# Kernel optimization log

Measured on AMD Instinct MI355X. Metric: run time of the kernel, lower is better.

Reference implementation:

```python
import jax, jax.numpy as jnp
import numpy as np
from jax.scipy.special import logsumexp

V, K, E, HD = 30000, 17, 128, 256
H = HD // 2  # per-direction hidden = 128
B, T = 128, 512


def setup_inputs() -> dict:
    key = jax.random.key(0)
    ks = jax.random.split(key, 16)
    s_e = 1.0 / np.sqrt(H)
    return {
        "input_ids": jax.random.randint(ks[0], (B, T), 0, V, dtype=jnp.int32),
        "tags": jax.random.randint(ks[1], (B, T), 0, K, dtype=jnp.int32),
        "mask": jnp.ones((B, T), dtype=bool),
        "embed_table": jax.random.normal(ks[2], (V, E), jnp.float32),
        "w_ih_f": jax.random.uniform(ks[3], (4 * H, E), jnp.float32, -s_e, s_e),
        "w_hh_f": jax.random.uniform(ks[4], (4 * H, H), jnp.float32, -s_e, s_e),
        "b_ih_f": jax.random.uniform(ks[5], (4 * H,), jnp.float32, -s_e, s_e),
        "b_hh_f": jax.random.uniform(ks[6], (4 * H,), jnp.float32, -s_e, s_e),
        "w_ih_b": jax.random.uniform(ks[7], (4 * H, E), jnp.float32, -s_e, s_e),
        "w_hh_b": jax.random.uniform(ks[8], (4 * H, H), jnp.float32, -s_e, s_e),
        "b_ih_b": jax.random.uniform(ks[9], (4 * H,), jnp.float32, -s_e, s_e),
        "b_hh_b": jax.random.uniform(ks[10], (4 * H,), jnp.float32, -s_e, s_e),
        "w_emit": jax.random.uniform(ks[11], (K, HD), jnp.float32, -s_e, s_e),
        "b_emit": jax.random.uniform(ks[12], (K,), jnp.float32, -s_e, s_e),
        "start_trans": jax.random.uniform(ks[13], (K,), jnp.float32, -0.1, 0.1),
        "end_trans": jax.random.uniform(ks[14], (K,), jnp.float32, -0.1, 0.1),
        "trans": jax.random.uniform(ks[15], (K, K), jnp.float32, -0.1, 0.1),
    }


def _lstm_dir(x, w_ih, w_hh, b_ih, b_hh):
    # x: [T, B, E] -> hs: [T, B, H]; PyTorch gate order i, f, g, o
    xp = jnp.einsum('tbe,ge->tbg', x, w_ih) + b_ih + b_hh  # [T,B,4H]
    h0 = jnp.zeros((x.shape[1], H), x.dtype)

    def step(carry, xpt):
        h, c = carry
        gates = xpt + h @ w_hh.T
        i, f, g, o = jnp.split(gates, 4, axis=-1)
        c = jax.nn.sigmoid(f) * c + jax.nn.sigmoid(i) * jnp.tanh(g)
        h = jax.nn.sigmoid(o) * jnp.tanh(c)
        return (h, c), h

    _, hs = jax.lax.scan(step, (h0, h0), xp)
    return hs


def _crf_nll_mean(emissions, tags, mask, start_trans, end_trans, trans):
    # emissions [B,T,K], tags [B,T] int, mask [B,T] bool; torchcrf reduction='mean'
    em_t = jnp.transpose(emissions, (1, 0, 2))      # [T,B,K]
    tags_t = tags.T                                  # [T,B]
    mask_t = mask.T                                  # [T,B]
    b_idx = jnp.arange(emissions.shape[0])
    mf = mask_t.astype(emissions.dtype)

    # numerator: score of the gold path
    score0 = start_trans[tags_t[0]] + em_t[0, b_idx, tags_t[0]]

    def num_step(carry, inp):
        score, prev = carry
        em, tg, m, mb = inp
        s = trans[prev, tg] + em[b_idx, tg]
        score = score + s * m
        prev = jnp.where(mb, tg, prev)
        return (score, prev), None

    (score, last_tag), _ = jax.lax.scan(
        num_step, (score0, tags_t[0]), (em_t[1:], tags_t[1:], mf[1:], mask_t[1:]))
    score = score + end_trans[last_tag]

    # denominator: forward algorithm (log partition)
    alpha0 = start_trans[None, :] + em_t[0]  # [B,K]

    def den_step(alpha, inp):
        em, mb = inp
        nxt = logsumexp(alpha[:, :, None] + trans[None, :, :] + em[:, None, :], axis=1)
        return jnp.where(mb[:, None], nxt, alpha), None

    alpha, _ = jax.lax.scan(den_step, alpha0, (em_t[1:], mask_t[1:]))
    logZ = logsumexp(alpha + end_trans[None, :], axis=1)

    llh = score - logZ
    return -jnp.mean(llh)


def reference(input_ids, tags, mask, embed_table,
              w_ih_f, w_hh_f, b_ih_f, b_hh_f,
              w_ih_b, w_hh_b, b_ih_b, b_hh_b,
              w_emit, b_emit, start_trans, end_trans, trans):
    x = embed_table[input_ids]                 # [B,T,E]
    xt = jnp.transpose(x, (1, 0, 2))           # [T,B,E]
    hs_f = _lstm_dir(xt, w_ih_f, w_hh_f, b_ih_f, b_hh_f)
    hs_b = _lstm_dir(xt[::-1], w_ih_b, w_hh_b, b_ih_b, b_hh_b)[::-1]
    h = jnp.concatenate([hs_f, hs_b], axis=-1)  # [T,B,2H]
    h = jnp.transpose(h, (1, 0, 2))             # [B,T,2H]
    emissions = jnp.einsum('bth,kh->btk', h, w_emit) + b_emit
    return _crf_nll_mean(emissions, tags, mask, start_trans, end_trans, trans)
```

## Files before the change

kernel.cpp:

```cpp
#include <hip/hip_runtime.h>
#include <hip/hip_bf16.h>


typedef __attribute__((ext_vector_type(8))) short short8;
typedef __attribute__((ext_vector_type(4))) float f32x4;
typedef __fp16 h2 __attribute__((ext_vector_type(2)));

__device__ __forceinline__ float bf2f(unsigned short u) {
    return __uint_as_float(((unsigned int)u) << 16);
}
__device__ __forceinline__ unsigned short f2bf(float f) {
    unsigned int x = __float_as_uint(f);
    x += 0x7FFFu + ((x >> 16) & 1u);
    return (unsigned short)(x >> 16);
}
__device__ __forceinline__ float sigf(float x) {
    return __builtin_amdgcn_rcpf(1.f + __expf(-x));
}
__device__ __forceinline__ float tanhf_(float x) {
    float e = __expf(-2.f * fabsf(x));
    float t = (1.f - e) * __builtin_amdgcn_rcpf(1.f + e);
    return copysignf(t, x);
}
__device__ __forceinline__ h2 i2h2(int x) { h2 r; __builtin_memcpy(&r, &x, 4); return r; }
__device__ __forceinline__ int h22i(h2 x) { int r; __builtin_memcpy(&r, &x, 4); return r; }

__device__ __forceinline__ float dot2acc(h2 a, h2 b, float c) {
#if __has_builtin(__builtin_amdgcn_fdot2)
    return __builtin_amdgcn_fdot2(a, b, c, false);
#else
    return fmaf((float)a.x, (float)b.x, fmaf((float)a.y, (float)b.y, c));
#endif
}

__global__ __launch_bounds__(256) void xp_gemm(
    const int* __restrict__ ids, const float* __restrict__ emb,
    const float* __restrict__ w_ih_f, const float* __restrict__ w_ih_b,
    const float* __restrict__ b_ih_f, const float* __restrict__ b_hh_f,
    const float* __restrict__ b_ih_b, const float* __restrict__ b_hh_b,
    unsigned short* __restrict__ xp)
{
    __shared__ unsigned short Ab[128][136];
    __shared__ unsigned short Wb[64][136];
    __shared__ unsigned short Cb[128][72];

    const int tid = threadIdx.x;
    const int m0  = blockIdx.x * 128;
    const int t   = m0 >> 7;

    {
        const int r = tid >> 1, half = tid & 1;
        const int id = ids[r * 512 + t];
        const float4* src = (const float4*)(emb + (long)id * 128 + half * 64);
        #pragma unroll
        for (int j = 0; j < 16; ++j) {
            float4 v = src[j];
            unsigned int p0 = (unsigned int)f2bf(v.x) | ((unsigned int)f2bf(v.y) << 16);
            unsigned int p1 = (unsigned int)f2bf(v.z) | ((unsigned int)f2bf(v.w) << 16);
            *(unsigned int*)&Ab[r][half*64 + j*4]     = p0;
            *(unsigned int*)&Ab[r][half*64 + j*4 + 2] = p1;
        }
    }

    const int w  = tid >> 6, l = tid & 63;
    const int lr = l & 15,  lg = l >> 4;

    for (int it = 0; it < 16; ++it) {
        const int n0 = it * 64;
        __syncthreads();
        {
            const int r = tid >> 2, q = tid & 3;
            const int g = n0 + r;
            const float* srcw = (g < 512) ? (w_ih_f + (long)g * 128)
                                          : (w_ih_b + (long)(g - 512) * 128);
            const float4* s4 = (const float4*)(srcw + q * 32);
            #pragma unroll
            for (int j = 0; j < 8; ++j) {
                float4 v = s4[j];
                unsigned int p0 = (unsigned int)f2bf(v.x) | ((unsigned int)f2bf(v.y) << 16);
                unsigned int p1 = (unsigned int)f2bf(v.z) | ((unsigned int)f2bf(v.w) << 16);
                *(unsigned int*)&Wb[r][q*32 + j*4]     = p0;
                *(unsigned int*)&Wb[r][q*32 + j*4 + 2] = p1;
            }
        }
        __syncthreads();

        f32x4 acc[2][4];
        #pragma unroll
        for (int a = 0; a < 2; ++a)
            #pragma unroll
            for (int c = 0; c < 4; ++c)
                acc[a][c] = (f32x4){0.f, 0.f, 0.f, 0.f};

        #pragma unroll
        for (int kk = 0; kk < 4; ++kk) {
            const int kb = kk * 32 + lg * 8;
            short8 af[2], bfr[4];
            #pragma unroll
            for (int mt2 = 0; mt2 < 2; ++mt2)
                af[mt2] = *(const short8*)&Ab[w*32 + mt2*16 + lr][kb];
            #pragma unroll
            for (int nt2 = 0; nt2 < 4; ++nt2)
                bfr[nt2] = *(const short8*)&Wb[nt2*16 + lr][kb];
            #pragma unroll
            for (int mt2 = 0; mt2 < 2; ++mt2)
                #pragma unroll
                for (int nt2 = 0; nt2 < 4; ++nt2)
                    acc[mt2][nt2] = __builtin_amdgcn_mfma_f32_16x16x32_bf16(
                        af[mt2], bfr[nt2], acc[mt2][nt2], 0, 0, 0);
        }

        #pragma unroll
        for (int nt2 = 0; nt2 < 4; ++nt2) {
            const int gc = n0 + nt2*16 + lr;
            const float bv = (gc < 512) ? (b_ih_f[gc] + b_hh_f[gc])
                                        : (b_ih_b[gc-512] + b_hh_b[gc-512]);
            #pragma unroll
            for (int mt2 = 0; mt2 < 2; ++mt2) {
                #pragma unroll
                for (int r = 0; r < 4; ++r) {
                    const int lrow = w*32 + mt2*16 + lg*4 + r;
                    Cb[lrow][nt2*16 + lr] = f2bf(acc[mt2][nt2][r] + bv);
                }
            }
        }
        __syncthreads();

        {
            const int rr = tid >> 1, hf = tid & 1;
            const int grow = m0 + rr;
            long dst;
            if (n0 < 512) {
                dst = (long)grow * 512 + n0 + hf*32;
            } else {
                const int tt = grow >> 7, bb = grow & 127;
                dst = 33554432L + (long)((511 - tt) * 128 + bb) * 512 + (n0 - 512) + hf*32;
            }
            const unsigned short* srcC = &Cb[rr][hf*32];
            unsigned short* dp = xp + dst;
            #pragma unroll
            for (int j = 0; j < 4; ++j)
                *(short8*)(dp + j*8) = *(const short8*)(srcC + j*8);
        }
    }
}

__global__ __launch_bounds__(256, 1) void lstm_rec(
    const unsigned short* __restrict__ xp,
    const float* __restrict__ w_hh_f, const float* __restrict__ w_hh_b,
    unsigned short* __restrict__ hbuf)
{
    const int tid = threadIdx.x;
    const int dir = blockIdx.x >> 7, b = blockIdx.x & 127;
    const float* whh = dir ? w_hh_b : w_hh_f;

    h2 w1p[64], w2p[64];
    #pragma unroll
    for (int j = 0; j < 16; ++j) {
        float4 a = *(const float4*)(whh + (long)tid * 128 + j*8);
        float4 c = *(const float4*)(whh + (long)tid * 128 + j*8 + 4);
        w1p[j*4+0] = __builtin_amdgcn_cvt_pkrtz(a.x, a.y);
        w1p[j*4+1] = __builtin_amdgcn_cvt_pkrtz(a.z, a.w);
        w1p[j*4+2] = __builtin_amdgcn_cvt_pkrtz(c.x, c.y);
        w1p[j*4+3] = __builtin_amdgcn_cvt_pkrtz(c.z, c.w);
    }
    #pragma unroll
    for (int j = 0; j < 16; ++j) {
        float4 a = *(const float4*)(whh + (long)(tid + 256) * 128 + j*8);
        float4 c = *(const float4*)(whh + (long)(tid + 256) * 128 + j*8 + 4);
        w2p[j*4+0] = __builtin_amdgcn_cvt_pkrtz(a.x, a.y);
        w2p[j*4+1] = __builtin_amdgcn_cvt_pkrtz(a.z, a.w);
        w2p[j*4+2] = __builtin_amdgcn_cvt_pkrtz(c.x, c.y);
        w2p[j*4+3] = __builtin_amdgcn_cvt_pkrtz(c.z, c.w);
    }

    __shared__ float gl[4][128];
    const int l   = tid & 63;
    const int u   = tid & 127;
    const int grp = tid >> 7;

    int hpi = 0;
    float cv0 = 0.f, cv1 = 0.f;
    const unsigned short* xpd = xp + (long)dir * 33554432L;

    unsigned short nxa = xpd[((long)0 * 128 + b) * 512 + tid];
    unsigned short nxb = xpd[((long)0 * 128 + b) * 512 + tid + 256];

    for (int t = 0; t < 512; ++t) {
        const float xpv1 = bf2f(nxa);
        const float xpv2 = bf2f(nxb);
        if (t < 511) {
            const unsigned short* nr = xpd + ((long)(t+1) * 128 + b) * 512;
            nxa = nr[tid];
            nxb = nr[tid + 256];
        }

        float acc1 = 0.f, acc2 = 0.f;
        #pragma unroll
        for (int j = 0; j < 64; ++j) {
            const h2 hj = i2h2(__builtin_amdgcn_readlane(hpi, j));
            acc1 = dot2acc(w1p[j], hj, acc1);
            acc2 = dot2acc(w2p[j], hj, acc2);
        }

        gl[grp][u]     = acc1 + xpv1;
        gl[2 + grp][u] = acc2 + xpv2;
        __syncthreads();

        const float2 iv = *(const float2*)&gl[0][2*l];
        const float2 fv = *(const float2*)&gl[1][2*l];
        const float2 gv = *(const float2*)&gl[2][2*l];
        const float2 ov = *(const float2*)&gl[3][2*l];
        cv0 = sigf(fv.x) * cv0 + sigf(iv.x) * tanhf_(gv.x);
        cv1 = sigf(fv.y) * cv1 + sigf(iv.y) * tanhf_(gv.y);
        const float h0 = sigf(ov.x) * tanhf_(cv0);
        const float h1 = sigf(ov.y) * tanhf_(cv1);
        hpi = h22i(__builtin_amdgcn_cvt_pkrtz(h0, h1));

        if (tid < 64) {
            const int tt = dir ? (511 - t) : t;
            unsigned short* hd = hbuf + ((long)b * 512 + tt) * 256 + dir * 128;
            *(unsigned int*)&hd[2*l] =
                (unsigned int)f2bf(h0) | ((unsigned int)f2bf(h1) << 16);
        }
        __syncthreads();
    }
}

__global__ __launch_bounds__(256) void emission(
    const unsigned short* __restrict__ hbuf, const float* __restrict__ w_emit,
    const float* __restrict__ b_emit, float* __restrict__ em)
{
    const int tid = threadIdx.x, w = tid >> 6, l = tid & 63;
    const int lr = l & 15, lg = l >> 4;
    const int m0 = blockIdx.x * 128;

    short8 bf[2][8];
    #pragma unroll
    for (int nt = 0; nt < 2; ++nt) {
        const int col = nt*16 + lr;
        #pragma unroll
        for (int kk = 0; kk < 8; ++kk) {
            short8 v = (short8){0,0,0,0,0,0,0,0};
            if (col < 17) {
                const float* s = w_emit + (long)col * 256 + kk*32 + lg*8;
                const float4 a = *(const float4*)s;
                const float4 c = *(const float4*)(s + 4);
                v[0] = (short)f2bf(a.x); v[1] = (short)f2bf(a.y);
                v[2] = (short)f2bf(a.z); v[3] = (short)f2bf(a.w);
                v[4] = (short)f2bf(c.x); v[5] = (short)f2bf(c.y);
                v[6] = (short)f2bf(c.z); v[7] = (short)f2bf(c.w);
            }
            bf[nt][kk] = v;
        }
    }

    f32x4 acc[2][2];
    #pragma unroll
    for (int a = 0; a < 2; ++a)
        #pragma unroll
        for (int c = 0; c < 2; ++c)
            acc[a][c] = (f32x4){0.f, 0.f, 0.f, 0.f};

    #pragma unroll
    for (int kk = 0; kk < 8; ++kk) {
        short8 af[2];
        #pragma unroll
        for (int mt = 0; mt < 2; ++mt) {
            const long row = m0 + w*32 + mt*16 + lr;
            af[mt] = *(const short8*)(hbuf + row * 256 + kk*32 + lg*8);
        }
        #pragma unroll
        for (int mt = 0; mt < 2; ++mt)
            #pragma unroll
            for (int nt = 0; nt < 2; ++nt)
                acc[mt][nt] = __builtin_amdgcn_mfma_f32_16x16x32_bf16(
                    af[mt], bf[nt][kk], acc[mt][nt], 0, 0, 0);
    }

    #pragma unroll
    for (int mt = 0; mt < 2; ++mt)
        #pragma unroll
        for (int nt = 0; nt < 2; ++nt) {
            const int col = nt*16 + lr;
            if (col < 17) {
                const float bb = b_emit[col];
                #pragma unroll
                for (int r = 0; r < 4; ++r) {
                    const long row = m0 + w*32 + mt*16 + lg*4 + r;
                    em[row * 17 + col] = acc[mt][nt][r] + bb;
                }
            }
        }
}

__global__ __launch_bounds__(64) void crf(
    const float* __restrict__ em, const int* __restrict__ tags,
    const float* __restrict__ start_t, const float* __restrict__ end_t,
    const float* __restrict__ trans, float* __restrict__ llh)
{
    const int b = blockIdx.x, l = threadIdx.x;
    const int* tg = tags + b * 512;
    const float* emb_ = em + (long)b * 512 * 17;

    float sc = 0.f;
    #pragma unroll
    for (int it = 0; it < 8; ++it) {
        const int t = it * 64 + l;
        const int cur = tg[t];
        float e = emb_[t * 17 + cur];
        float tr = (t > 0) ? trans[tg[t-1] * 17 + cur] : 0.f;
        sc += e + tr;
    }
    #pragma unroll
    for (int m = 32; m >= 1; m >>= 1) sc += __shfl_xor(sc, m, 64);

    const bool act = (l < 17);
    const int j = act ? l : 16;

    float eT[17];
    #pragma unroll
    for (int i = 0; i < 17; ++i) eT[i] = __expf(trans[i * 17 + j]);

    float v0 = act ? (start_t[j] + emb_[j]) : -1e30f;
    float m0 = v0;
    #pragma unroll
    for (int m = 32; m >= 1; m >>= 1) m0 = fmaxf(m0, __shfl_xor(m0, m, 64));
    float al = act ? __expf(v0 - m0) : 0.f;
    float accl = m0;

    float em_next = emb_[17 + j];
    for (int t = 1; t < 512; ++t) {
        const float emv = em_next;
        if (t + 1 < 512) em_next = emb_[(t + 1) * 17 + j];
        float s = 0.f;
        #pragma unroll
        for (int i = 0; i < 17; ++i) {
            const float ai = __int_as_float(
                __builtin_amdgcn_readlane(__float_as_int(al), i));
            s = fmaf(ai, eT[i], s);
        }
        al = act ? s * __expf(emv) : 0.f;
        if ((t & 3) == 0) {
            float mx = al;
            #pragma unroll
            for (int m = 32; m >= 1; m >>= 1) mx = fmaxf(mx, __shfl_xor(mx, m, 64));
            al = al * __builtin_amdgcn_rcpf(mx);
            accl += __logf(mx);
        }
    }
    float fin = act ? al * __expf(end_t[j]) : 0.f;
    #pragma unroll
    for (int m = 32; m >= 1; m >>= 1) fin += __shfl_xor(fin, m, 64);
    const float logZ = __logf(fin) + accl;

    if (l == 0) {
        sc += start_t[tg[0]] + end_t[tg[511]];
        llh[b] = sc - logZ;
    }
}

__global__ __launch_bounds__(64) void finalize(
    const float* __restrict__ llh, float* __restrict__ out)
{
    const int l = threadIdx.x;
    float s = llh[l] + llh[l + 64];
    #pragma unroll
    for (int m = 32; m >= 1; m >>= 1) s += __shfl_xor(s, m, 64);
    if (l == 0) out[0] = -s * (1.f / 128.f);
}

extern "C" void kernel_launch(void* const* d_in, const int* in_sizes, int n_in,
                              void* d_out, int out_size, void* d_ws, size_t ws_size,
                              hipStream_t stream) {
    (void)in_sizes; (void)n_in; (void)out_size; (void)ws_size;
    const int*   ids    = (const int*)d_in[0];
    const int*   tags   = (const int*)d_in[1];
    const float* emb    = (const float*)d_in[3];
    const float* w_ih_f = (const float*)d_in[4];
    const float* w_hh_f = (const float*)d_in[5];
    const float* b_ih_f = (const float*)d_in[6];
    const float* b_hh_f = (const float*)d_in[7];
    const float* w_ih_b = (const float*)d_in[8];
    const float* w_hh_b = (const float*)d_in[9];
    const float* b_ih_b = (const float*)d_in[10];
    const float* b_hh_b = (const float*)d_in[11];
    const float* w_emit = (const float*)d_in[12];
    const float* b_emit = (const float*)d_in[13];
    const float* st     = (const float*)d_in[14];
    const float* en     = (const float*)d_in[15];
    const float* tr     = (const float*)d_in[16];

    char* ws = (char*)d_ws;
    unsigned short* xp   = (unsigned short*)(ws);
    unsigned short* hbuf = (unsigned short*)(ws + 134217728L);
    float*          em   = (float*)(ws + 167772160L);
    float*          llh  = (float*)(ws + 172228608L);
    float*          out  = (float*)d_out;

    xp_gemm<<<dim3(512), dim3(256), 0, stream>>>(ids, emb, w_ih_f, w_ih_b,
                                                 b_ih_f, b_hh_f, b_ih_b, b_hh_b, xp);
    lstm_rec<<<dim3(256), dim3(256), 0, stream>>>(xp, w_hh_f, w_hh_b, hbuf);
    emission<<<dim3(512), dim3(256), 0, stream>>>(hbuf, w_emit, b_emit, em);
    crf<<<dim3(128), dim3(64), 0, stream>>>(em, tags, st, en, tr, llh);
    finalize<<<dim3(1), dim3(64), 0, stream>>>(llh, out);
}
```

Measured before the change: 816.2 us.

## Pack two LSTM sequences per block and double-buffer gate LDS to drop a barrier

The recurrent LSTM kernel now runs two independent sequences per 512-thread block (128 blocks instead of 256) and double-buffers the shared gate array by timestep parity. This lets it remove the second __syncthreads per step. The aim is to halve the barriers per step and use fewer CUs. The trade-off is that the two sequences' waves now wait on each other at every barrier, and launch_bounds(512,2) may constrain the register budget for the 128 packed weights per thread.

```diff
diff --git a/kernel.cpp b/kernel.cpp
--- a/kernel.cpp
+++ b/kernel.cpp
@@ -145,20 +145,23 @@
     }
 }
 
-__global__ __launch_bounds__(256, 1) void lstm_rec(
+__global__ __launch_bounds__(512, 2) void lstm_rec(
     const unsigned short* __restrict__ xp,
     const float* __restrict__ w_hh_f, const float* __restrict__ w_hh_b,
     unsigned short* __restrict__ hbuf)
 {
-    const int tid = threadIdx.x;
-    const int dir = blockIdx.x >> 7, b = blockIdx.x & 127;
+    const int tid  = threadIdx.x;
+    const int s    = tid >> 8;
+    const int stid = tid & 255;
+    const int seq  = blockIdx.x * 2 + s;
+    const int dir  = seq >> 7, b = seq & 127;
     const float* whh = dir ? w_hh_b : w_hh_f;
 
     h2 w1p[64], w2p[64];
     #pragma unroll
     for (int j = 0; j < 16; ++j) {
-        float4 a = *(const float4*)(whh + (long)tid * 128 + j*8);
-        float4 c = *(const float4*)(whh + (long)tid * 128 + j*8 + 4);
+        float4 a = *(const float4*)(whh + (long)stid * 128 + j*8);
+        float4 c = *(const float4*)(whh + (long)stid * 128 + j*8 + 4);
         w1p[j*4+0] = __builtin_amdgcn_cvt_pkrtz(a.x, a.y);
         w1p[j*4+1] = __builtin_amdgcn_cvt_pkrtz(a.z, a.w);
         w1p[j*4+2] = __builtin_amdgcn_cvt_pkrtz(c.x, c.y);
@@ -166,33 +169,34 @@
     }
     #pragma unroll
     for (int j = 0; j < 16; ++j) {
-        float4 a = *(const float4*)(whh + (long)(tid + 256) * 128 + j*8);
-        float4 c = *(const float4*)(whh + (long)(tid + 256) * 128 + j*8 + 4);
+        float4 a = *(const float4*)(whh + (long)(stid + 256) * 128 + j*8);
+        float4 c = *(const float4*)(whh + (long)(stid + 256) * 128 + j*8 + 4);
         w2p[j*4+0] = __builtin_amdgcn_cvt_pkrtz(a.x, a.y);
         w2p[j*4+1] = __builtin_amdgcn_cvt_pkrtz(a.z, a.w);
         w2p[j*4+2] = __builtin_amdgcn_cvt_pkrtz(c.x, c.y);
         w2p[j*4+3] = __builtin_amdgcn_cvt_pkrtz(c.z, c.w);
     }
 
-    __shared__ float gl[4][128];
-    const int l   = tid & 63;
-    const int u   = tid & 127;
-    const int grp = tid >> 7;
+    __shared__ float gl[2][2][4][128];
+    const int l   = stid & 63;
+    const int u   = stid & 127;
+    const int grp = stid >> 7;
 
     int hpi = 0;
     float cv0 = 0.f, cv1 = 0.f;
     const unsigned short* xpd = xp + (long)dir * 33554432L;
 
-    unsigned short nxa = xpd[((long)0 * 128 + b) * 512 + tid];
-    unsigned short nxb = xpd[((long)0 * 128 + b) * 512 + tid + 256];
+    unsigned short nxa = xpd[((long)0 * 128 + b) * 512 + stid];
+    unsigned short nxb = xpd[((long)0 * 128 + b) * 512 + stid + 256];
 
     for (int t = 0; t < 512; ++t) {
+        const int p = t & 1;
         const float xpv1 = bf2f(nxa);
         const float xpv2 = bf2f(nxb);
         if (t < 511) {
             const unsigned short* nr = xpd + ((long)(t+1) * 128 + b) * 512;
-            nxa = nr[tid];
-            nxb = nr[tid + 256];
+            nxa = nr[stid];
+            nxb = nr[stid + 256];
         }
 
         float acc1 = 0.f, acc2 = 0.f;
@@ -203,27 +207,26 @@
             acc2 = dot2acc(w2p[j], hj, acc2);
         }
 
-        gl[grp][u]     = acc1 + xpv1;
-        gl[2 + grp][u] = acc2 + xpv2;
+        gl[s][p][grp][u]     = acc1 + xpv1;
+        gl[s][p][2 + grp][u] = acc2 + xpv2;
         __syncthreads();
 
-        const float2 iv = *(const float2*)&gl[0][2*l];
-        const float2 fv = *(const float2*)&gl[1][2*l];
-        const float2 gv = *(const float2*)&gl[2][2*l];
-        const float2 ov = *(const float2*)&gl[3][2*l];
+        const float2 iv = *(const float2*)&gl[s][p][0][2*l];
+        const float2 fv = *(const float2*)&gl[s][p][1][2*l];
+        const float2 gv = *(const float2*)&gl[s][p][2][2*l];
+        const float2 ov = *(const float2*)&gl[s][p][3][2*l];
         cv0 = sigf(fv.x) * cv0 + sigf(iv.x) * tanhf_(gv.x);
         cv1 = sigf(fv.y) * cv1 + sigf(iv.y) * tanhf_(gv.y);
         const float h0 = sigf(ov.x) * tanhf_(cv0);
         const float h1 = sigf(ov.y) * tanhf_(cv1);
         hpi = h22i(__builtin_amdgcn_cvt_pkrtz(h0, h1));
 
-        if (tid < 64) {
+        if (stid < 64) {
             const int tt = dir ? (511 - t) : t;
             unsigned short* hd = hbuf + ((long)b * 512 + tt) * 256 + dir * 128;
             *(unsigned int*)&hd[2*l] =
                 (unsigned int)f2bf(h0) | ((unsigned int)f2bf(h1) << 16);
         }
-        __syncthreads();
     }
 }
 
@@ -400,7 +403,7 @@
 
     xp_gemm<<<dim3(512), dim3(256), 0, stream>>>(ids, emb, w_ih_f, w_ih_b,
                                                  b_ih_f, b_hh_f, b_ih_b, b_hh_b, xp);
-    lstm_rec<<<dim3(256), dim3(256), 0, stream>>>(xp, w_hh_f, w_hh_b, hbuf);
+    lstm_rec<<<dim3(128), dim3(512), 0, stream>>>(xp, w_hh_f, w_hh_b, hbuf);
     emission<<<dim3(512), dim3(256), 0, stream>>>(hbuf, w_emit, b_emit, em);
     crf<<<dim3(128), dim3(64), 0, stream>>>(em, tags, st, en, tr, llh);
     finalize<<<dim3(1), dim3(64), 0, stream>>>(llh, out);
```

Result: slower. 985.5 us (+20.7%).

## Double-buffer LSTM gate exchange to drop one barrier per timestep

Applied to the files above, without the earlier changes.

The recurrent LSTM kernel now ping-pongs the shared gate buffer across timesteps, which removes the second __syncthreads per step. It also changes the hidden-unit ownership (lane l handles units l and l+64) and packs the weights to match, so all four gates of a unit sit in one float4 slot. The dot-product loop uses two accumulators per output to shorten the dependency chain, and the launch-bounds occupancy hint is raised to 2. In exchange, hbuf is written with two scalar 16-bit stores instead of one 32-bit store, and the higher occupancy hint may limit registers for the 128 packed weights per thread.

```diff
diff --git a/kernel.cpp b/kernel.cpp
--- a/kernel.cpp
+++ b/kernel.cpp
@@ -145,7 +145,7 @@
     }
 }
 
-__global__ __launch_bounds__(256, 1) void lstm_rec(
+__global__ __launch_bounds__(256, 2) void lstm_rec(
     const unsigned short* __restrict__ xp,
     const float* __restrict__ w_hh_f, const float* __restrict__ w_hh_b,
     unsigned short* __restrict__ hbuf)
@@ -156,37 +156,39 @@
 
     h2 w1p[64], w2p[64];
     #pragma unroll
-    for (int j = 0; j < 16; ++j) {
-        float4 a = *(const float4*)(whh + (long)tid * 128 + j*8);
-        float4 c = *(const float4*)(whh + (long)tid * 128 + j*8 + 4);
-        w1p[j*4+0] = __builtin_amdgcn_cvt_pkrtz(a.x, a.y);
-        w1p[j*4+1] = __builtin_amdgcn_cvt_pkrtz(a.z, a.w);
-        w1p[j*4+2] = __builtin_amdgcn_cvt_pkrtz(c.x, c.y);
-        w1p[j*4+3] = __builtin_amdgcn_cvt_pkrtz(c.z, c.w);
-    }
-    #pragma unroll
-    for (int j = 0; j < 16; ++j) {
-        float4 a = *(const float4*)(whh + (long)(tid + 256) * 128 + j*8);
-        float4 c = *(const float4*)(whh + (long)(tid + 256) * 128 + j*8 + 4);
-        w2p[j*4+0] = __builtin_amdgcn_cvt_pkrtz(a.x, a.y);
-        w2p[j*4+1] = __builtin_amdgcn_cvt_pkrtz(a.z, a.w);
-        w2p[j*4+2] = __builtin_amdgcn_cvt_pkrtz(c.x, c.y);
-        w2p[j*4+3] = __builtin_amdgcn_cvt_pkrtz(c.z, c.w);
-    }
-
-    __shared__ float gl[4][128];
-    const int l   = tid & 63;
-    const int u   = tid & 127;
-    const int grp = tid >> 7;
-
+    for (int jj = 0; jj < 16; ++jj) {
+        float4 a = *(const float4*)(whh + (long)tid * 128 + jj*4);
+        float4 c = *(const float4*)(whh + (long)tid * 128 + 64 + jj*4);
+        w1p[jj*4+0] = __builtin_amdgcn_cvt_pkrtz(a.x, c.x);
+        w1p[jj*4+1] = __builtin_amdgcn_cvt_pkrtz(a.y, c.y);
+        w1p[jj*4+2] = __builtin_amdgcn_cvt_pkrtz(a.z, c.z);
+        w1p[jj*4+3] = __builtin_amdgcn_cvt_pkrtz(a.w, c.w);
+    }
+    #pragma unroll
+    for (int jj = 0; jj < 16; ++jj) {
+        float4 a = *(const float4*)(whh + (long)(tid + 256) * 128 + jj*4);
+        float4 c = *(const float4*)(whh + (long)(tid + 256) * 128 + 64 + jj*4);
+        w2p[jj*4+0] = __builtin_amdgcn_cvt_pkrtz(a.x, c.x);
+        w2p[jj*4+1] = __builtin_amdgcn_cvt_pkrtz(a.y, c.y);
+        w2p[jj*4+2] = __builtin_amdgcn_cvt_pkrtz(a.z, c.z);
+        w2p[jj*4+3] = __builtin_amdgcn_cvt_pkrtz(a.w, c.w);
+    }
+
+    __shared__ float glx[2][128][4];
+
+    const int l    = tid & 63;
+    const int u    = tid & 127;
+    const int half = tid >> 7;
+
+    float cv0 = 0.f, cv1 = 0.f;
     int hpi = 0;
-    float cv0 = 0.f, cv1 = 0.f;
     const unsigned short* xpd = xp + (long)dir * 33554432L;
 
     unsigned short nxa = xpd[((long)0 * 128 + b) * 512 + tid];
     unsigned short nxb = xpd[((long)0 * 128 + b) * 512 + tid + 256];
 
     for (int t = 0; t < 512; ++t) {
+        const int p = t & 1;
         const float xpv1 = bf2f(nxa);
         const float xpv2 = bf2f(nxb);
         if (t < 511) {
@@ -195,35 +197,36 @@
             nxb = nr[tid + 256];
         }
 
-        float acc1 = 0.f, acc2 = 0.f;
-        #pragma unroll
-        for (int j = 0; j < 64; ++j) {
-            const h2 hj = i2h2(__builtin_amdgcn_readlane(hpi, j));
-            acc1 = dot2acc(w1p[j], hj, acc1);
-            acc2 = dot2acc(w2p[j], hj, acc2);
-        }
-
-        gl[grp][u]     = acc1 + xpv1;
-        gl[2 + grp][u] = acc2 + xpv2;
+        float a1a = 0.f, a1b = 0.f, a2a = 0.f, a2b = 0.f;
+        #pragma unroll
+        for (int j = 0; j < 64; j += 2) {
+            const h2 hj0 = i2h2(__builtin_amdgcn_readlane(hpi, j));
+            const h2 hj1 = i2h2(__builtin_amdgcn_readlane(hpi, j + 1));
+            a1a = dot2acc(w1p[j],     hj0, a1a);
+            a2a = dot2acc(w2p[j],     hj0, a2a);
+            a1b = dot2acc(w1p[j + 1], hj1, a1b);
+            a2b = dot2acc(w2p[j + 1], hj1, a2b);
+        }
+        const float g1 = a1a + a1b + xpv1;
+        const float g2 = a2a + a2b + xpv2;
+
+        *(float2*)&glx[p][u][half * 2] = make_float2(g1, g2);
         __syncthreads();
 
-        const float2 iv = *(const float2*)&gl[0][2*l];
-        const float2 fv = *(const float2*)&gl[1][2*l];
-        const float2 gv = *(const float2*)&gl[2][2*l];
-        const float2 ov = *(const float2*)&gl[3][2*l];
-        cv0 = sigf(fv.x) * cv0 + sigf(iv.x) * tanhf_(gv.x);
-        cv1 = sigf(fv.y) * cv1 + sigf(iv.y) * tanhf_(gv.y);
-        const float h0 = sigf(ov.x) * tanhf_(cv0);
-        const float h1 = sigf(ov.y) * tanhf_(cv1);
+        const float4 q0 = *(const float4*)&glx[p][l][0];
+        const float4 q1 = *(const float4*)&glx[p][l + 64][0];
+        cv0 = sigf(q0.z) * cv0 + sigf(q0.x) * tanhf_(q0.y);
+        cv1 = sigf(q1.z) * cv1 + sigf(q1.x) * tanhf_(q1.y);
+        const float h0 = sigf(q0.w) * tanhf_(cv0);
+        const float h1 = sigf(q1.w) * tanhf_(cv1);
         hpi = h22i(__builtin_amdgcn_cvt_pkrtz(h0, h1));
 
         if (tid < 64) {
             const int tt = dir ? (511 - t) : t;
             unsigned short* hd = hbuf + ((long)b * 512 + tt) * 256 + dir * 128;
-            *(unsigned int*)&hd[2*l] =
-                (unsigned int)f2bf(h0) | ((unsigned int)f2bf(h1) << 16);
-        }
-        __syncthreads();
+            hd[l]      = f2bf(h0);
+            hd[l + 64] = f2bf(h1);
+        }
     }
 }
 
```

New measurement: 729.8 us. -10.6%, faster.

## Split LSTM gate rows across 512 threads with double-buffered LDS; unroll CRF

Applied to the files above, without the earlier changes.

The recurrent LSTM kernel now runs 512 threads per block, each owning one gate row (64 packed weights) instead of two. This halves the serial dot-product chain per thread, and two independent accumulators add ILP. Gate results go to a parity double-buffered shared array, which removes the second barrier per time step. The CRF forward loop is unrolled by four with renormalization once per group and emissions prefetched four ahead. The cost is more waves and barrier participants per step, and double buffering relies on the next step's barrier ordering reads before overwrites.

```diff
diff --git a/kernel.cpp b/kernel.cpp
--- a/kernel.cpp
+++ b/kernel.cpp
@@ -145,7 +145,7 @@
     }
 }
 
-__global__ __launch_bounds__(256, 1) void lstm_rec(
+__global__ __launch_bounds__(512, 2) void lstm_rec(
     const unsigned short* __restrict__ xp,
     const float* __restrict__ w_hh_f, const float* __restrict__ w_hh_b,
     unsigned short* __restrict__ hbuf)
@@ -154,63 +154,52 @@
     const int dir = blockIdx.x >> 7, b = blockIdx.x & 127;
     const float* whh = dir ? w_hh_b : w_hh_f;
 
-    h2 w1p[64], w2p[64];
-    #pragma unroll
-    for (int j = 0; j < 16; ++j) {
-        float4 a = *(const float4*)(whh + (long)tid * 128 + j*8);
-        float4 c = *(const float4*)(whh + (long)tid * 128 + j*8 + 4);
-        w1p[j*4+0] = __builtin_amdgcn_cvt_pkrtz(a.x, a.y);
-        w1p[j*4+1] = __builtin_amdgcn_cvt_pkrtz(a.z, a.w);
-        w1p[j*4+2] = __builtin_amdgcn_cvt_pkrtz(c.x, c.y);
-        w1p[j*4+3] = __builtin_amdgcn_cvt_pkrtz(c.z, c.w);
-    }
-    #pragma unroll
-    for (int j = 0; j < 16; ++j) {
-        float4 a = *(const float4*)(whh + (long)(tid + 256) * 128 + j*8);
-        float4 c = *(const float4*)(whh + (long)(tid + 256) * 128 + j*8 + 4);
-        w2p[j*4+0] = __builtin_amdgcn_cvt_pkrtz(a.x, a.y);
-        w2p[j*4+1] = __builtin_amdgcn_cvt_pkrtz(a.z, a.w);
-        w2p[j*4+2] = __builtin_amdgcn_cvt_pkrtz(c.x, c.y);
-        w2p[j*4+3] = __builtin_amdgcn_cvt_pkrtz(c.z, c.w);
-    }
-
-    __shared__ float gl[4][128];
-    const int l   = tid & 63;
-    const int u   = tid & 127;
-    const int grp = tid >> 7;
-
+    h2 wp[64];
+    #pragma unroll
+    for (int jj = 0; jj < 16; ++jj) {
+        float4 a = *(const float4*)(whh + (long)tid * 128 + jj*8);
+        float4 c = *(const float4*)(whh + (long)tid * 128 + jj*8 + 4);
+        wp[jj*4+0] = __builtin_amdgcn_cvt_pkrtz(a.x, a.y);
+        wp[jj*4+1] = __builtin_amdgcn_cvt_pkrtz(a.z, a.w);
+        wp[jj*4+2] = __builtin_amdgcn_cvt_pkrtz(c.x, c.y);
+        wp[jj*4+3] = __builtin_amdgcn_cvt_pkrtz(c.z, c.w);
+    }
+
+    __shared__ float gl[2][4][128];
+
+    const int l    = tid & 63;
+    const int gate = tid >> 7;
+    const int unit = tid & 127;
+
+    float cv0 = 0.f, cv1 = 0.f;
     int hpi = 0;
-    float cv0 = 0.f, cv1 = 0.f;
     const unsigned short* xpd = xp + (long)dir * 33554432L;
 
-    unsigned short nxa = xpd[((long)0 * 128 + b) * 512 + tid];
-    unsigned short nxb = xpd[((long)0 * 128 + b) * 512 + tid + 256];
+    unsigned short nx = xpd[((long)0 * 128 + b) * 512 + tid];
 
     for (int t = 0; t < 512; ++t) {
-        const float xpv1 = bf2f(nxa);
-        const float xpv2 = bf2f(nxb);
+        const int p = t & 1;
+        const float xpv = bf2f(nx);
         if (t < 511) {
-            const unsigned short* nr = xpd + ((long)(t+1) * 128 + b) * 512;
-            nxa = nr[tid];
-            nxb = nr[tid + 256];
-        }
-
-        float acc1 = 0.f, acc2 = 0.f;
-        #pragma unroll
-        for (int j = 0; j < 64; ++j) {
-            const h2 hj = i2h2(__builtin_amdgcn_readlane(hpi, j));
-            acc1 = dot2acc(w1p[j], hj, acc1);
-            acc2 = dot2acc(w2p[j], hj, acc2);
-        }
-
-        gl[grp][u]     = acc1 + xpv1;
-        gl[2 + grp][u] = acc2 + xpv2;
+            nx = xpd[((long)(t+1) * 128 + b) * 512 + tid];
+        }
+
+        float accA = 0.f, accB = 0.f;
+        #pragma unroll
+        for (int j = 0; j < 64; j += 2) {
+            const h2 hj0 = i2h2(__builtin_amdgcn_readlane(hpi, j));
+            const h2 hj1 = i2h2(__builtin_amdgcn_readlane(hpi, j + 1));
+            accA = dot2acc(wp[j],     hj0, accA);
+            accB = dot2acc(wp[j + 1], hj1, accB);
+        }
+
+        gl[p][gate][unit] = accA + accB + xpv;
         __syncthreads();
 
-        const float2 iv = *(const float2*)&gl[0][2*l];
-        const float2 fv = *(const float2*)&gl[1][2*l];
-        const float2 gv = *(const float2*)&gl[2][2*l];
-        const float2 ov = *(const float2*)&gl[3][2*l];
+        const float2 iv = *(const float2*)&gl[p][0][2*l];
+        const float2 fv = *(const float2*)&gl[p][1][2*l];
+        const float2 gv = *(const float2*)&gl[p][2][2*l];
+        const float2 ov = *(const float2*)&gl[p][3][2*l];
         cv0 = sigf(fv.x) * cv0 + sigf(iv.x) * tanhf_(gv.x);
         cv1 = sigf(fv.y) * cv1 + sigf(iv.y) * tanhf_(gv.y);
         const float h0 = sigf(ov.x) * tanhf_(cv0);
@@ -223,7 +212,6 @@
             *(unsigned int*)&hd[2*l] =
                 (unsigned int)f2bf(h0) | ((unsigned int)f2bf(h1) << 16);
         }
-        __syncthreads();
     }
 }
 
@@ -329,10 +317,7 @@
     float al = act ? __expf(v0 - m0) : 0.f;
     float accl = m0;
 
-    float em_next = emb_[17 + j];
-    for (int t = 1; t < 512; ++t) {
-        const float emv = em_next;
-        if (t + 1 < 512) em_next = emb_[(t + 1) * 17 + j];
+    auto stepf = [&](float emv) {
         float s = 0.f;
         #pragma unroll
         for (int i = 0; i < 17; ++i) {
@@ -341,14 +326,24 @@
             s = fmaf(ai, eT[i], s);
         }
         al = act ? s * __expf(emv) : 0.f;
-        if ((t & 3) == 0) {
-            float mx = al;
-            #pragma unroll
-            for (int m = 32; m >= 1; m >>= 1) mx = fmaxf(mx, __shfl_xor(mx, m, 64));
-            al = al * __builtin_amdgcn_rcpf(mx);
-            accl += __logf(mx);
-        }
-    }
+    };
+
+    float e0 = emb_[1*17 + j], e1 = emb_[2*17 + j];
+    float e2 = emb_[3*17 + j], e3 = emb_[4*17 + j];
+
+    for (int t = 1; t <= 505; t += 4) {
+        stepf(e0); e0 = emb_[(t+4)*17 + j];
+        stepf(e1); e1 = emb_[(t+5)*17 + j];
+        stepf(e2); e2 = emb_[(t+6)*17 + j];
+        stepf(e3); e3 = (t+7 < 512) ? emb_[(t+7)*17 + j] : 0.f;
+        float mx = al;
+        #pragma unroll
+        for (int m = 32; m >= 1; m >>= 1) mx = fmaxf(mx, __shfl_xor(mx, m, 64));
+        al = al * __builtin_amdgcn_rcpf(mx);
+        accl += __logf(mx);
+    }
+    stepf(e0); stepf(e1); stepf(e2);
+
     float fin = act ? al * __expf(end_t[j]) : 0.f;
     #pragma unroll
     for (int m = 32; m >= 1; m >>= 1) fin += __shfl_xor(fin, m, 64);
@@ -400,7 +395,7 @@
 
     xp_gemm<<<dim3(512), dim3(256), 0, stream>>>(ids, emb, w_ih_f, w_ih_b,
                                                  b_ih_f, b_hh_f, b_ih_b, b_hh_b, xp);
-    lstm_rec<<<dim3(256), dim3(256), 0, stream>>>(xp, w_hh_f, w_hh_b, hbuf);
+    lstm_rec<<<dim3(256), dim3(512), 0, stream>>>(xp, w_hh_f, w_hh_b, hbuf);
     emission<<<dim3(512), dim3(256), 0, stream>>>(hbuf, w_emit, b_emit, em);
     crf<<<dim3(128), dim3(64), 0, stream>>>(em, tags, st, en, tr, llh);
     finalize<<<dim3(1), dim3(64), 0, stream>>>(llh, out);
```

Result: faster. 748.7 us (-8.3%).
